# Optimization experiments

Hardware: AMD Instinct MI355X
Metric: run time of the kernel (lower is better)

The kernel has to match this reference:

```python
import jax, jax.numpy as jnp
import numpy as np

D_MODEL = 1024
BATCH = 8
SEQ = 2048
LN_EPS = 1e-5


def setup_inputs() -> dict:
    key = jax.random.key(0)
    ks = jax.random.split(key, 8)
    scale = 0.1 / np.sqrt(D_MODEL)
    x = jax.random.normal(ks[0], (BATCH, SEQ, D_MODEL), dtype=jnp.float32)
    return {
        "x": x,
        "ln_w": jnp.ones((D_MODEL,), jnp.float32),
        "ln_b": jnp.zeros((D_MODEL,), jnp.float32),
        # layer_idx=0, n_layers=4 -> ratio_1 = 1.0 (init), perturb slightly for a non-trivial mix
        "tmk": jnp.ones((D_MODEL,), jnp.float32) * 0.9,
        "tmv": jnp.ones((D_MODEL,), jnp.float32) * 0.9,
        "tmr": jnp.ones((D_MODEL,), jnp.float32) * 0.9,
        "decay_w": jnp.full((D_MODEL,), -0.5, jnp.float32)
        + 0.1 * jax.random.normal(ks[1], (D_MODEL,), jnp.float32),
        "Wk": scale * jax.random.normal(ks[2], (D_MODEL, D_MODEL), jnp.float32),
        "Wv": scale * jax.random.normal(ks[3], (D_MODEL, D_MODEL), jnp.float32),
        "Wr": scale * jax.random.normal(ks[4], (D_MODEL, D_MODEL), jnp.float32),
        "Wo": scale * jax.random.normal(ks[5], (D_MODEL, D_MODEL), jnp.float32),
    }


def _layernorm(z, w, b):
    m = jnp.mean(z, axis=-1, keepdims=True)
    v = jnp.mean(jnp.square(z - m), axis=-1, keepdims=True)
    return (z - m) * jax.lax.rsqrt(v + LN_EPS) * w + b


def reference(x, ln_w, ln_b, tmk, tmv, tmr, decay_w, Wk, Wv, Wr, Wo):
    # x: (B, T, D)
    xn = _layernorm(x, ln_w, ln_b)
    # prev_x at t=0 is zeros (not LN of zeros), afterwards LN(x_{t-1})
    prev = jnp.pad(xn[:, :-1, :], ((0, 0), (1, 0), (0, 0)))
    xk = xn * tmk + prev * (1.0 - tmk)
    xv = xn * tmv + prev * (1.0 - tmv)
    xr = xn * tmr + prev * (1.0 - tmr)
    k = jnp.einsum("btd,ed->bte", xk, Wk)
    v = jnp.einsum("btd,ed->bte", xv, Wv)
    r = jax.nn.sigmoid(jnp.einsum("btd,ed->bte", xr, Wr))
    decay = jax.nn.sigmoid(decay_w)  # (D,)

    kv = (k * v).swapaxes(0, 1)  # (T, B, D) time-major for scan

    def step(S, kv_t):
        S_new = decay * S + kv_t
        return S_new, S_new

    S0 = jnp.zeros((x.shape[0], x.shape[2]), x.dtype)
    final_S, S_seq = jax.lax.scan(step, S0, kv)
    S_seq = S_seq.swapaxes(0, 1)  # (B, T, D)

    out = x + r * jnp.einsum("btd,ed->bte", S_seq, Wo)
    return out, final_S, S_seq
```

## Files before the change

### kernel.cpp

```cpp
#include <hip/hip_runtime.h>
#include <cstdint>

#define D_MODEL 1024
#define SEQ 2048
#define BATCH 8
#define M_TOTAL (BATCH*SEQ)
#define NC 64
#define CL (SEQ/NC)

typedef float f32x4 __attribute__((ext_vector_type(4)));
typedef short bf16x8 __attribute__((ext_vector_type(8)));
typedef unsigned short u16x4 __attribute__((ext_vector_type(4)));

__device__ __forceinline__ float b2f(unsigned short s){
  union { float f; unsigned u; } z; z.u = ((unsigned)s) << 16; return z.f;
}
__device__ __forceinline__ unsigned short f2b(float f){
  union { float f; unsigned u; } z; z.f = f;
  unsigned u = z.u;
  u += 0x7fffu + ((u >> 16) & 1u);
  return (unsigned short)(u >> 16);
}
__device__ __forceinline__ float sigmoidf_(float v){
  return 1.0f / (1.0f + __expf(-v));
}
__device__ __forceinline__ void gld_lds16(const void* g, void* l){
  __builtin_amdgcn_global_load_lds((const __attribute__((address_space(1))) unsigned int*)g,
                                   (__attribute__((address_space(3))) unsigned int*)l,
                                   16, 0, 0);
}

__device__ __forceinline__ void swz_mn(int bid, int& m0, int& n0){
  int xcd = bid & 7;
  int loc = bid >> 3;
  int wg  = xcd*64 + loc;
  m0 = (wg >> 3) * 256;
  n0 = (wg & 7) * 128;
}

__global__ __launch_bounds__(256) void prep_kernel(const float* __restrict__ x,
                                                   const float* __restrict__ lnw, const float* __restrict__ lnb,
                                                   const float* __restrict__ tmk, const float* __restrict__ tmv,
                                                   const float* __restrict__ tmr,
                                                   unsigned short* __restrict__ XK, unsigned short* __restrict__ XV,
                                                   unsigned short* __restrict__ XR,
                                                   const float* __restrict__ W0, const float* __restrict__ W1,
                                                   const float* __restrict__ W2, const float* __restrict__ W3,
                                                   unsigned short* __restrict__ WC){
  int tid = threadIdx.x;
  if (blockIdx.x >= M_TOTAL/8){
    int t = blockIdx.x - M_TOTAL/8;
    int mat = t >> 10;
    const float* src = (mat==0) ? W0 : (mat==1) ? W1 : (mat==2) ? W2 : W3;
    size_t i = ((size_t)(t & 1023)*256 + tid)*4;
    f32x4 v = *(const f32x4*)(src + i);
    u16x4 o; o[0]=f2b(v[0]); o[1]=f2b(v[1]); o[2]=f2b(v[2]); o[3]=f2b(v[3]);
    *(u16x4*)(WC + (size_t)mat*1048576 + i) = o;
    return;
  }
  int r0 = blockIdx.x * 8;
  bool seqfirst = (r0 & (SEQ-1)) == 0;
  size_t col = (size_t)tid*4;

  f32x4 xr[9];
  float s1[9], s2[9];
  #pragma unroll
  for (int i=0;i<9;i++){
    if (i==0 && seqfirst){
      xr[0][0]=0.f; xr[0][1]=0.f; xr[0][2]=0.f; xr[0][3]=0.f;
    } else {
      xr[i] = *(const f32x4*)(x + (size_t)(r0-1+i)*D_MODEL + col);
    }
    s1[i] = xr[i][0]+xr[i][1]+xr[i][2]+xr[i][3];
    s2[i] = xr[i][0]*xr[i][0]+xr[i][1]*xr[i][1]+xr[i][2]*xr[i][2]+xr[i][3]*xr[i][3];
  }
  #pragma unroll
  for (int off = 32; off > 0; off >>= 1){
    #pragma unroll
    for (int i=0;i<9;i++){
      s1[i] += __shfl_xor(s1[i], off);
      s2[i] += __shfl_xor(s2[i], off);
    }
  }
  __shared__ float red[4][18];
  int w = tid >> 6, lane = tid & 63;
  if (lane == 0){
    #pragma unroll
    for (int i=0;i<9;i++){ red[w][i]=s1[i]; red[w][9+i]=s2[i]; }
  }
  __syncthreads();
  float mean[9], rstd[9];
  #pragma unroll
  for (int i=0;i<9;i++){
    float a = red[0][i]+red[1][i]+red[2][i]+red[3][i];
    float b = red[0][9+i]+red[1][9+i]+red[2][9+i]+red[3][9+i];
    mean[i] = a*(1.0f/1024.0f);
    float var = b*(1.0f/1024.0f) - mean[i]*mean[i];
    rstd[i] = rsqrtf(var + 1e-5f);
  }

  f32x4 wv = *(const f32x4*)(lnw + col);
  f32x4 bv = *(const f32x4*)(lnb + col);
  f32x4 k4 = *(const f32x4*)(tmk + col);
  f32x4 v4 = *(const f32x4*)(tmv + col);
  f32x4 r4 = *(const f32x4*)(tmr + col);

  f32x4 np;
  if (seqfirst){ np[0]=0.f; np[1]=0.f; np[2]=0.f; np[3]=0.f; }
  else {
    #pragma unroll
    for (int j=0;j<4;j++) np[j] = (xr[0][j]-mean[0])*rstd[0]*wv[j] + bv[j];
  }
  #pragma unroll
  for (int i=0;i<8;i++){
    f32x4 nc;
    #pragma unroll
    for (int j=0;j<4;j++) nc[j] = (xr[i+1][j]-mean[i+1])*rstd[i+1]*wv[j] + bv[j];
    u16x4 ok, ov, orr;
    #pragma unroll
    for (int j=0;j<4;j++){
      ok[j]  = f2b(np[j] + k4[j]*(nc[j]-np[j]));
      ov[j]  = f2b(np[j] + v4[j]*(nc[j]-np[j]));
      orr[j] = f2b(np[j] + r4[j]*(nc[j]-np[j]));
    }
    size_t base = (size_t)(r0+i)*D_MODEL + col;
    *(u16x4*)(XK + base) = ok;
    *(u16x4*)(XV + base) = ov;
    *(u16x4*)(XR + base) = orr;
    np = nc;
  }
}

__device__ __forceinline__ void gemm256_core(const unsigned short* __restrict__ A,
                                             const unsigned short* __restrict__ W,
                                             int m0, int n0, int tid,
                                             unsigned short* As, unsigned short* Bs,
                                             f32x4 (&acc)[8][4]){
  int wid = tid >> 6, lane = tid & 63;
  int wm = wid >> 1, wn = wid & 1;
  int fr = lane & 15, fg = lane >> 4;

  int offAg[8], offBg[4];
  #pragma unroll
  for (int it = 0; it < 8; ++it){
    int chunk = it*256 + tid;
    int row = chunk >> 3;
    int cg = (chunk & 7) ^ (row & 7);
    offAg[it] = (m0+row)*D_MODEL + cg*8;
  }
  #pragma unroll
  for (int it = 0; it < 4; ++it){
    int chunk = it*256 + tid;
    int row = chunk >> 3;
    int cg = (chunk & 7) ^ (row & 7);
    offBg[it] = (n0+row)*D_MODEL + cg*8;
  }

  #define STAGE(kt_) { \
    _Pragma("unroll") \
    for (int it = 0; it < 8; ++it) \
      gld_lds16(A + offAg[it] + (kt_)*64, &As[(it*256+tid)*8]); \
    _Pragma("unroll") \
    for (int it = 0; it < 4; ++it) \
      gld_lds16(W + offBg[it] + (kt_)*64, &Bs[(it*256+tid)*8]); \
  }

  STAGE(0);

  bf16x8 aL[4][2], aH[4][2], bL[2][2], bH[2][2];

  #pragma unroll 1
  for (int kt = 0; kt < 16; ++kt){
    asm volatile("s_waitcnt vmcnt(0)" ::: "memory");
    __builtin_amdgcn_s_barrier();
    asm volatile("" ::: "memory");

    #pragma unroll
    for (int mi=0; mi<4; ++mi)
      #pragma unroll
      for (int ks=0; ks<2; ++ks){
        int r = wm*128 + mi*16 + fr;
        aL[mi][ks] = *(const bf16x8*)(&As[r*64 + (((ks*4+fg)^(r&7))<<3)]);
      }
    #pragma unroll
    for (int ni=0; ni<2; ++ni)
      #pragma unroll
      for (int ks=0; ks<2; ++ks){
        int r = wn*64 + ni*16 + fr;
        bL[ni][ks] = *(const bf16x8*)(&Bs[r*64 + (((ks*4+fg)^(r&7))<<3)]);
      }
    __builtin_amdgcn_s_barrier();
    asm volatile("s_waitcnt lgkmcnt(0)" ::: "memory");
    __builtin_amdgcn_s_setprio(1);
    #pragma unroll
    for (int mi=0; mi<4; ++mi)
      #pragma unroll
      for (int ni=0; ni<2; ++ni)
        #pragma unroll
        for (int ks=0; ks<2; ++ks)
          acc[mi][ni] = __builtin_amdgcn_mfma_f32_16x16x32_bf16(aL[mi][ks], bL[ni][ks], acc[mi][ni], 0, 0, 0);
    __builtin_amdgcn_s_setprio(0);
    __builtin_amdgcn_s_barrier();

    #pragma unroll
    for (int ni=0; ni<2; ++ni)
      #pragma unroll
      for (int ks=0; ks<2; ++ks){
        int r = wn*64 + (ni+2)*16 + fr;
        bH[ni][ks] = *(const bf16x8*)(&Bs[r*64 + (((ks*4+fg)^(r&7))<<3)]);
      }
    __builtin_amdgcn_s_barrier();
    asm volatile("s_waitcnt lgkmcnt(0)" ::: "memory");
    __builtin_amdgcn_s_setprio(1);
    #pragma unroll
    for (int mi=0; mi<4; ++mi)
      #pragma unroll
      for (int ni=0; ni<2; ++ni)
        #pragma unroll
        for (int ks=0; ks<2; ++ks)
          acc[mi][ni+2] = __builtin_amdgcn_mfma_f32_16x16x32_bf16(aL[mi][ks], bH[ni][ks], acc[mi][ni+2], 0, 0, 0);
    __builtin_amdgcn_s_setprio(0);
    __builtin_amdgcn_s_barrier();

    #pragma unroll
    for (int mi=0; mi<4; ++mi)
      #pragma unroll
      for (int ks=0; ks<2; ++ks){
        int r = wm*128 + (mi+4)*16 + fr;
        aH[mi][ks] = *(const bf16x8*)(&As[r*64 + (((ks*4+fg)^(r&7))<<3)]);
      }
    asm volatile("s_waitcnt lgkmcnt(0)" ::: "memory");
    __builtin_amdgcn_s_barrier();
    asm volatile("" ::: "memory");

    if (kt < 15) STAGE(kt+1);

    __builtin_amdgcn_s_setprio(1);
    #pragma unroll
    for (int mi=0; mi<4; ++mi)
      #pragma unroll
      for (int ni=0; ni<2; ++ni)
        #pragma unroll
        for (int ks=0; ks<2; ++ks)
          acc[mi+4][ni+2] = __builtin_amdgcn_mfma_f32_16x16x32_bf16(aH[mi][ks], bH[ni][ks], acc[mi+4][ni+2], 0, 0, 0);
    #pragma unroll
    for (int mi=0; mi<4; ++mi)
      #pragma unroll
      for (int ni=0; ni<2; ++ni)
        #pragma unroll
        for (int ks=0; ks<2; ++ks)
          acc[mi+4][ni] = __builtin_amdgcn_mfma_f32_16x16x32_bf16(aH[mi][ks], bL[ni][ks], acc[mi+4][ni], 0, 0, 0);
    __builtin_amdgcn_s_setprio(0);
  }
  #undef STAGE
}

__global__ __launch_bounds__(256, 2) void gemm_kr_kernel(const unsigned short* __restrict__ XK,
                                                         const unsigned short* __restrict__ XR,
                                                         const unsigned short* __restrict__ Wk,
                                                         const unsigned short* __restrict__ Wr,
                                                         unsigned short* __restrict__ KB,
                                                         unsigned short* __restrict__ RB){
  __shared__ alignas(16) unsigned short As[16384];
  __shared__ alignas(16) unsigned short Bs[8192];
  int m0, n0; swz_mn(blockIdx.x, m0, n0);
  int z = blockIdx.z;
  int tid = threadIdx.x;
  const unsigned short* A = z ? XR : XK;
  const unsigned short* W = z ? Wr : Wk;
  unsigned short* O       = z ? RB : KB;

  f32x4 acc[8][4];
  #pragma unroll
  for (int i=0;i<8;i++)
    #pragma unroll
    for (int j=0;j<4;j++){ acc[i][j][0]=0.f; acc[i][j][1]=0.f; acc[i][j][2]=0.f; acc[i][j][3]=0.f; }

  gemm256_core(A, W, m0, n0, tid, As, Bs, acc);

  int wid = tid >> 6, lane = tid & 63;
  int wm = wid >> 1, wn = wid & 1;
  int fr = lane & 15, fg = lane >> 4;
  #pragma unroll
  for (int mi=0; mi<8; ++mi){
    #pragma unroll
    for (int ni=0; ni<4; ++ni){
      int c = n0 + wn*64 + ni*16 + fr;
      #pragma unroll
      for (int j=0; j<4; ++j){
        int r = m0 + wm*128 + mi*16 + fg*4 + j;
        size_t idx = (size_t)r*D_MODEL + c;
        float val = acc[mi][ni][j];
        if (z) val = sigmoidf_(val);
        O[idx] = f2b(val);
      }
    }
  }
}

__global__ __launch_bounds__(256, 2) void gemm_v_kernel(const unsigned short* __restrict__ XV,
                                                        const unsigned short* __restrict__ Wv,
                                                        unsigned short* __restrict__ KB){
  __shared__ alignas(16) unsigned short As[16384];
  __shared__ alignas(16) unsigned short Bs[8192];
  int m0, n0; swz_mn(blockIdx.x, m0, n0);
  int tid = threadIdx.x;

  f32x4 acc[8][4];
  #pragma unroll
  for (int i=0;i<8;i++)
    #pragma unroll
    for (int j=0;j<4;j++){ acc[i][j][0]=0.f; acc[i][j][1]=0.f; acc[i][j][2]=0.f; acc[i][j][3]=0.f; }

  gemm256_core(XV, Wv, m0, n0, tid, As, Bs, acc);

  int wid = tid >> 6, lane = tid & 63;
  int wm = wid >> 1, wn = wid & 1;
  int fr = lane & 15, fg = lane >> 4;
  #pragma unroll
  for (int mi=0; mi<8; ++mi){
    #pragma unroll
    for (int ni=0; ni<4; ++ni){
      int c = n0 + wn*64 + ni*16 + fr;
      #pragma unroll
      for (int j=0; j<4; ++j){
        int r = m0 + wm*128 + mi*16 + fg*4 + j;
        size_t idx = (size_t)r*D_MODEL + c;
        KB[idx] = f2b(acc[mi][ni][j] * b2f(KB[idx]));
      }
    }
  }
}

__global__ __launch_bounds__(256, 2) void gemm_out_kernel(const unsigned short* __restrict__ Sb,
                                                          const unsigned short* __restrict__ Wo,
                                                          const float* __restrict__ x,
                                                          const unsigned short* __restrict__ RB,
                                                          float* __restrict__ out){
  __shared__ alignas(16) unsigned short As[16384];
  __shared__ alignas(16) unsigned short Bs[8192];
  int m0, n0; swz_mn(blockIdx.x, m0, n0);
  int tid = threadIdx.x;

  f32x4 acc[8][4];
  #pragma unroll
  for (int i=0;i<8;i++)
    #pragma unroll
    for (int j=0;j<4;j++){ acc[i][j][0]=0.f; acc[i][j][1]=0.f; acc[i][j][2]=0.f; acc[i][j][3]=0.f; }

  gemm256_core(Sb, Wo, m0, n0, tid, As, Bs, acc);

  int wid = tid >> 6, lane = tid & 63;
  int wm = wid >> 1, wn = wid & 1;
  int fr = lane & 15, fg = lane >> 4;
  #pragma unroll
  for (int mi=0; mi<8; ++mi){
    #pragma unroll
    for (int ni=0; ni<4; ++ni){
      int c = n0 + wn*64 + ni*16 + fr;
      #pragma unroll
      for (int j=0; j<4; ++j){
        int r = m0 + wm*128 + mi*16 + fg*4 + j;
        size_t idx = (size_t)r*D_MODEL + c;
        float rr = b2f(RB[idx]);
        out[idx] = x[idx] + rr * acc[mi][ni][j];
      }
    }
  }
}

__global__ __launch_bounds__(256) void scan_p1_kernel(const unsigned short* __restrict__ kv,
                                                      const float* __restrict__ dw,
                                                      float* __restrict__ carr){
  int bc = blockIdx.x;
  int b = bc >> 6, c = bc & (NC-1);
  int d0 = threadIdx.x * 4;
  float dx = sigmoidf_(dw[d0+0]);
  float dy = sigmoidf_(dw[d0+1]);
  float dz = sigmoidf_(dw[d0+2]);
  float dwv = sigmoidf_(dw[d0+3]);
  float Sx=0.f, Sy=0.f, Sz=0.f, Sw=0.f;
  size_t base = ((size_t)(b*SEQ + c*CL))*D_MODEL + d0;
  for (int i=0;i<CL;i++){
    u16x4 k4 = *(const u16x4*)(kv + base);
    Sx = dx*Sx + b2f(k4[0]);
    Sy = dy*Sy + b2f(k4[1]);
    Sz = dz*Sz + b2f(k4[2]);
    Sw = dwv*Sw + b2f(k4[3]);
    base += D_MODEL;
  }
  f32x4 o; o[0]=Sx; o[1]=Sy; o[2]=Sz; o[3]=Sw;
  *(f32x4*)(carr + (size_t)bc*D_MODEL + d0) = o;
}

__global__ __launch_bounds__(256) void scan_p2_kernel(const float* __restrict__ dw, float* __restrict__ carr){
  int gid = blockIdx.x*256 + threadIdx.x;
  int b = gid >> 10, d = gid & (D_MODEL-1);
  float dec = sigmoidf_(dw[d]);
  float dL = dec;
  #pragma unroll
  for (int i=0;i<5;i++) dL *= dL;
  float S = 0.f;
  for (int c=0;c<NC;c++){
    size_t idx = ((size_t)(b*NC + c))*D_MODEL + d;
    float cr = carr[idx];
    carr[idx] = S;
    S = dL*S + cr;
  }
}

__global__ __launch_bounds__(256) void scan_p3_kernel(const unsigned short* __restrict__ kv,
                                                      const float* __restrict__ dw,
                                                      const float* __restrict__ cin,
                                                      float* __restrict__ sseq,
                                                      float* __restrict__ finalS,
                                                      unsigned short* __restrict__ sb16){
  int bc = blockIdx.x;
  int b = bc >> 6, c = bc & (NC-1);
  int d0 = threadIdx.x * 4;
  float dx = sigmoidf_(dw[d0+0]);
  float dy = sigmoidf_(dw[d0+1]);
  float dz = sigmoidf_(dw[d0+2]);
  float dwv = sigmoidf_(dw[d0+3]);
  f32x4 S = *(const f32x4*)(cin + (size_t)bc*D_MODEL + d0);
  size_t base = ((size_t)(b*SEQ + c*CL))*D_MODEL + d0;
  for (int i=0;i<CL;i++){
    u16x4 k4 = *(const u16x4*)(kv + base);
    S[0] = dx*S[0] + b2f(k4[0]);
    S[1] = dy*S[1] + b2f(k4[1]);
    S[2] = dz*S[2] + b2f(k4[2]);
    S[3] = dwv*S[3] + b2f(k4[3]);
    *(f32x4*)(sseq + base) = S;
    u16x4 s4; s4[0]=f2b(S[0]); s4[1]=f2b(S[1]); s4[2]=f2b(S[2]); s4[3]=f2b(S[3]);
    *(u16x4*)(sb16 + base) = s4;
    base += D_MODEL;
  }
  if (c == NC-1)
    *(f32x4*)(finalS + (size_t)b*D_MODEL + d0) = S;
}

extern "C" void kernel_launch(void* const* d_in, const int* in_sizes, int n_in,
                              void* d_out, int out_size, void* d_ws, size_t ws_size,
                              hipStream_t stream){
  const float* x   = (const float*)d_in[0];
  const float* lnw = (const float*)d_in[1];
  const float* lnb = (const float*)d_in[2];
  const float* tmk = (const float*)d_in[3];
  const float* tmv = (const float*)d_in[4];
  const float* tmr = (const float*)d_in[5];
  const float* dw  = (const float*)d_in[6];
  const float* Wk  = (const float*)d_in[7];
  const float* Wv  = (const float*)d_in[8];
  const float* Wr  = (const float*)d_in[9];
  const float* Wo  = (const float*)d_in[10];

  float* out    = (float*)d_out;
  float* finalS = out + (size_t)M_TOTAL*D_MODEL;
  float* sseq   = finalS + (size_t)BATCH*D_MODEL;

  unsigned short* XK = (unsigned short*)d_out;
  unsigned short* XV = (unsigned short*)((char*)d_out + 33554432);
  unsigned short* XR = (unsigned short*)sseq;

  char* w = (char*)d_ws;
  unsigned short* WC   = (unsigned short*)(w + 0);
  unsigned short* SB16 = (unsigned short*)(w + 8388608);
  unsigned short* KB   = (unsigned short*)(w + 41943040);
  unsigned short* RB   = (unsigned short*)(w + 75497472);
  float*          CARR = (float*)(w + 109051904);

  prep_kernel<<<M_TOTAL/8 + 4096, 256, 0, stream>>>(x, lnw, lnb, tmk, tmv, tmr, XK, XV, XR,
                                                    Wk, Wv, Wr, Wo, WC);

  gemm_kr_kernel<<<dim3(512,1,2), 256, 0, stream>>>(XK, XR, WC, WC + (size_t)2*1048576, KB, RB);
  gemm_v_kernel<<<512, 256, 0, stream>>>(XV, WC + (size_t)1048576, KB);

  scan_p1_kernel<<<BATCH*NC, 256, 0, stream>>>(KB, dw, CARR);
  scan_p2_kernel<<<32, 256, 0, stream>>>(dw, CARR);
  scan_p3_kernel<<<BATCH*NC, 256, 0, stream>>>(KB, dw, CARR, sseq, finalS, SB16);

  gemm_out_kernel<<<512, 256, 0, stream>>>(SB16, WC + (size_t)3*1048576, x, RB, out);
}
```

Baseline: 244.2 us.

## Load full LDS fragments once per k-step and issue all MFMAs together

Replaces the four-phase ping-pong schedule, which interleaved partial LDS fragment loads with MFMA groups across several barriers, with a single pass. Each k-step now loads all A and B fragments into registers, waits once, barriers, issues the next global-to-LDS stage, then runs all 64 MFMAs. This removes several barriers and waitcnts per iteration and lets the next tile's loads overlap the whole MFMA block. It raises register pressure (all fragments live at once) under launch bounds (256,2) and loses the LDS/MFMA interleaving inside an iteration.

```diff
diff --git a/kernel.cpp b/kernel.cpp
--- a/kernel.cpp
+++ b/kernel.cpp
@@ -167,7 +167,7 @@
 
   STAGE(0);
 
-  bf16x8 aL[4][2], aH[4][2], bL[2][2], bH[2][2];
+  bf16x8 a[8][2], b[4][2];
 
   #pragma unroll 1
   for (int kt = 0; kt < 16; ++kt){
@@ -176,80 +176,35 @@
     asm volatile("" ::: "memory");
 
     #pragma unroll
-    for (int mi=0; mi<4; ++mi)
+    for (int mi=0; mi<8; ++mi)
       #pragma unroll
       for (int ks=0; ks<2; ++ks){
         int r = wm*128 + mi*16 + fr;
-        aL[mi][ks] = *(const bf16x8*)(&As[r*64 + (((ks*4+fg)^(r&7))<<3)]);
+        a[mi][ks] = *(const bf16x8*)(&As[r*64 + (((ks*4+fg)^(r&7))<<3)]);
       }
     #pragma unroll
-    for (int ni=0; ni<2; ++ni)
+    for (int ni=0; ni<4; ++ni)
       #pragma unroll
       for (int ks=0; ks<2; ++ks){
         int r = wn*64 + ni*16 + fr;
-        bL[ni][ks] = *(const bf16x8*)(&Bs[r*64 + (((ks*4+fg)^(r&7))<<3)]);
+        b[ni][ks] = *(const bf16x8*)(&Bs[r*64 + (((ks*4+fg)^(r&7))<<3)]);
       }
+
+    asm volatile("s_waitcnt lgkmcnt(0)" ::: "memory");
+    __builtin_amdgcn_sched_barrier(0);
     __builtin_amdgcn_s_barrier();
-    asm volatile("s_waitcnt lgkmcnt(0)" ::: "memory");
+    asm volatile("" ::: "memory");
+
+    if (kt < 15) STAGE(kt+1);
+
     __builtin_amdgcn_s_setprio(1);
     #pragma unroll
-    for (int mi=0; mi<4; ++mi)
-      #pragma unroll
-      for (int ni=0; ni<2; ++ni)
+    for (int mi=0; mi<8; ++mi)
+      #pragma unroll
+      for (int ni=0; ni<4; ++ni)
         #pragma unroll
         for (int ks=0; ks<2; ++ks)
-          acc[mi][ni] = __builtin_amdgcn_mfma_f32_16x16x32_bf16(aL[mi][ks], bL[ni][ks], acc[mi][ni], 0, 0, 0);
-    __builtin_amdgcn_s_setprio(0);
-    __builtin_amdgcn_s_barrier();
-
-    #pragma unroll
-    for (int ni=0; ni<2; ++ni)
-      #pragma unroll
-      for (int ks=0; ks<2; ++ks){
-        int r = wn*64 + (ni+2)*16 + fr;
-        bH[ni][ks] = *(const bf16x8*)(&Bs[r*64 + (((ks*4+fg)^(r&7))<<3)]);
-      }
-    __builtin_amdgcn_s_barrier();
-    asm volatile("s_waitcnt lgkmcnt(0)" ::: "memory");
-    __builtin_amdgcn_s_setprio(1);
-    #pragma unroll
-    for (int mi=0; mi<4; ++mi)
-      #pragma unroll
-      for (int ni=0; ni<2; ++ni)
-        #pragma unroll
-        for (int ks=0; ks<2; ++ks)
-          acc[mi][ni+2] = __builtin_amdgcn_mfma_f32_16x16x32_bf16(aL[mi][ks], bH[ni][ks], acc[mi][ni+2], 0, 0, 0);
-    __builtin_amdgcn_s_setprio(0);
-    __builtin_amdgcn_s_barrier();
-
-    #pragma unroll
-    for (int mi=0; mi<4; ++mi)
-      #pragma unroll
-      for (int ks=0; ks<2; ++ks){
-        int r = wm*128 + (mi+4)*16 + fr;
-        aH[mi][ks] = *(const bf16x8*)(&As[r*64 + (((ks*4+fg)^(r&7))<<3)]);
-      }
-    asm volatile("s_waitcnt lgkmcnt(0)" ::: "memory");
-    __builtin_amdgcn_s_barrier();
-    asm volatile("" ::: "memory");
-
-    if (kt < 15) STAGE(kt+1);
-
-    __builtin_amdgcn_s_setprio(1);
-    #pragma unroll
-    for (int mi=0; mi<4; ++mi)
-      #pragma unroll
-      for (int ni=0; ni<2; ++ni)
-        #pragma unroll
-        for (int ks=0; ks<2; ++ks)
-          acc[mi+4][ni+2] = __builtin_amdgcn_mfma_f32_16x16x32_bf16(aH[mi][ks], bH[ni][ks], acc[mi+4][ni+2], 0, 0, 0);
-    #pragma unroll
-    for (int mi=0; mi<4; ++mi)
-      #pragma unroll
-      for (int ni=0; ni<2; ++ni)
-        #pragma unroll
-        for (int ks=0; ks<2; ++ks)
-          acc[mi+4][ni] = __builtin_amdgcn_mfma_f32_16x16x32_bf16(aH[mi][ks], bL[ni][ks], acc[mi+4][ni], 0, 0, 0);
+          acc[mi][ni] = __builtin_amdgcn_mfma_f32_16x16x32_bf16(a[mi][ks], b[ni][ks], acc[mi][ni], 0, 0, 0);
     __builtin_amdgcn_s_setprio(0);
   }
   #undef STAGE
```

Result: slower. 254.0 us (+4.0%).
